# Optimization experiments

Hardware: AMD Instinct MI355X
Metric: run time of the kernel (lower is better)

## Reference

```python
import jax, jax.numpy as jnp
import numpy as np

B, S, D, H, R = 16, 2048, 1024, 1024, 16


def setup_inputs() -> dict:
    key = jax.random.key(0)
    ks = jax.random.split(key, 6)
    inv = 1.0 / np.sqrt(D)
    return {
        "x": jax.random.normal(ks[0], (B, S, D), jnp.float32),
        "Wa": jax.random.uniform(ks[1], (H, D), jnp.float32, -inv, inv),
        "ba": jnp.zeros((H,), jnp.float32),
        "Wg": jax.random.uniform(ks[2], (R, D), jnp.float32, -inv, inv),
        "bg": jnp.zeros((R,), jnp.float32),
        "Wu": jax.random.uniform(ks[3], (H, D), jnp.float32, -inv, inv),
        "bu": jnp.zeros((H,), jnp.float32),
        "u": jax.random.normal(ks[4], (H, R), jnp.float32) * 0.02,
        "v": jax.random.normal(ks[5], (H, R), jnp.float32) * 0.02,
    }


def reference(x, Wa, ba, Wg, bg, Wu, bu, u, v):
    # Precompute all per-step projections in big GEMMs (same math as the
    # per-step Linear calls in the original loop).
    a = jax.nn.sigmoid(jnp.einsum('bsd,hd->bsh', x, Wa) + ba)   # [B,S,H]
    g = jnp.einsum('bsd,rd->bsr', x, Wg) + bg                    # [B,S,R]
    u_in = jnp.einsum('bsd,hd->bsh', x, Wu) + bu                 # [B,S,H]

    def step(state, ins):
        a_t, g_t, u_t = ins                      # [B,H], [B,R], [B,H]
        low_rank = (state @ v) * g_t             # [B,R]
        state = a_t * state + u_t + low_rank @ u.T
        return state, None

    init = jnp.zeros((x.shape[0], Wa.shape[0]), x.dtype)
    seq = (jnp.swapaxes(a, 0, 1), jnp.swapaxes(g, 0, 1), jnp.swapaxes(u_in, 0, 1))
    state, _ = jax.lax.scan(step, init, seq)
    return state  # [B, H]
```

## Files before the change

kernel.cpp:

```cpp
#include <hip/hip_runtime.h>
#include <hip/hip_bf16.h>
#include <stdint.h>

#define Bb 16
#define Ss 2048
#define Dd 1024
#define Hh 1024
#define Rr 16
#define Mm 32768

typedef __attribute__((ext_vector_type(4))) float f32x4;
typedef __attribute__((ext_vector_type(8))) short bf16x8;
typedef __attribute__((ext_vector_type(2))) _Float16 h2;

__device__ __forceinline__ unsigned short f2bf(float f) {
    union { float f; uint32_t u; } c; c.f = f;
    uint32_t u = c.u + 0x7fffu + ((c.u >> 16) & 1u);
    return (unsigned short)(u >> 16);
}
__device__ __forceinline__ float bfbits2f(uint32_t bits) {
    union { uint32_t u; float f; } c; c.u = bits << 16; return c.f;
}
__device__ __forceinline__ h2 u2h(unsigned int x) {
    union { unsigned int u; h2 h; } c; c.u = x; return c.h;
}
__device__ __forceinline__ h2 mkh2(float a, float b) {
    h2 r; r.x = (_Float16)a; r.y = (_Float16)b; return r;
}

__device__ __forceinline__ float DOT2(h2 a, h2 b, float c) {
#if __has_builtin(__builtin_amdgcn_fdot2)
    return __builtin_amdgcn_fdot2(a, b, c, false);
#else
    return fmaf((float)a.x, (float)b.x, fmaf((float)a.y, (float)b.y, c));
#endif
}

__device__ __forceinline__ float dpp_xor8(float x) {
    return __int_as_float(__builtin_amdgcn_mov_dpp(
        __float_as_int(x), 0x128, 0xF, 0xF, false));
}
__device__ __forceinline__ float dpp_xor1(float x) {
    return __int_as_float(__builtin_amdgcn_mov_dpp(
        __float_as_int(x), 0xB1, 0xF, 0xF, false));
}

__device__ __forceinline__ void gld16(const void* gsrc, void* ldst) {
    __builtin_amdgcn_global_load_lds(
        (const __attribute__((address_space(1))) unsigned int*)gsrc,
        (__attribute__((address_space(3))) unsigned int*)ldst, 16, 0, 0);
}

__device__ __forceinline__ void softbar() {
    __asm volatile("" ::: "memory");
    __builtin_amdgcn_s_waitcnt(0xC07F);
    __builtin_amdgcn_s_barrier();
    __asm volatile("" ::: "memory");
}

__global__ __launch_bounds__(256) void k_convert(
    const float* __restrict__ x, const float* __restrict__ Wa,
    const float* __restrict__ Wu,
    unsigned short* __restrict__ xb, unsigned short* __restrict__ Wab,
    unsigned short* __restrict__ Wub)
{
    long e = ((long)blockIdx.x * 256 + threadIdx.x) * 4;
    const long nx = (long)Mm * Dd;
    const long nw = (long)Hh * Dd;
    const float* src; unsigned short* dst; long o;
    if (e < nx)            { src = x;  dst = xb;  o = e; }
    else if (e < nx + nw)  { src = Wa; dst = Wab; o = e - nx; }
    else                   { src = Wu; dst = Wub; o = e - nx - nw; }
    float4 f = *(const float4*)(src + o);
    ushort4 r;
    r.x = f2bf(f.x); r.y = f2bf(f.y); r.z = f2bf(f.z); r.w = f2bf(f.w);
    *(ushort4*)(dst + o) = r;
}

__global__ __launch_bounds__(256) void k_gemm(
    const unsigned short* __restrict__ Xb,
    const unsigned short* __restrict__ Wab,
    const unsigned short* __restrict__ Wub,
    const float* __restrict__ ba, const float* __restrict__ bu,
    unsigned short* __restrict__ outA, unsigned short* __restrict__ outU)
{
    __shared__ short At[128 * 32];
    __shared__ short Bt[128 * 32];

    const int tid  = threadIdx.x;
    const int lane = tid & 63;
    const int wave = tid >> 6;
    const int bm = blockIdx.x;
    const int bn = blockIdx.y;
    const int region = bn >> 3;
    const int nbase = (bn & 7) * 128;

    const short* Ag = (const short*)Xb;
    const short* Bg = (const short*)(region ? Wub : Wab);
    const float* bias = region ? bu : ba;
    unsigned short* outp = region ? outU : outA;

    const int wm = wave & 1, wn = wave >> 1;
    const int srow = lane >> 2, sseg = lane & 3;
    const int mrow = lane & 15, kb = lane >> 4;

    f32x4 acc[4][4] = {};

    for (int kt = 0; kt < 32; ++kt) {
        __syncthreads();
        const int k0 = kt * 32;
        #pragma unroll
        for (int p = 0; p < 2; ++p) {
            const int row = p * 64 + wave * 16 + srow;
            const short* ga = Ag + (long)(bm * 128 + row) * Dd + k0 + sseg * 8;
            gld16((const void*)ga, (void*)&At[p * 2048 + wave * 512]);
            const short* gb = Bg + (long)(nbase + row) * Dd + k0 + sseg * 8;
            gld16((const void*)gb, (void*)&Bt[p * 2048 + wave * 512]);
        }
        __syncthreads();

        bf16x8 af[4], bq[4];
        #pragma unroll
        for (int i = 0; i < 4; ++i) {
            af[i] = *(const bf16x8*)&At[(wm * 64 + i * 16 + mrow) * 32 + kb * 8];
            bq[i] = *(const bf16x8*)&Bt[(wn * 64 + i * 16 + mrow) * 32 + kb * 8];
        }
        #pragma unroll
        for (int i = 0; i < 4; ++i)
            #pragma unroll
            for (int j = 0; j < 4; ++j)
                acc[i][j] = __builtin_amdgcn_mfma_f32_16x16x32_bf16(
                    af[i], bq[j], acc[i][j], 0, 0, 0);
    }

    const int col = lane & 15, rq = lane >> 4;
    #pragma unroll
    for (int j = 0; j < 4; ++j) {
        const int n = nbase + wn * 64 + j * 16 + col;
        const float bv = bias[n];
        #pragma unroll
        for (int i = 0; i < 4; ++i) {
            const int mb = bm * 128 + wm * 64 + i * 16 + rq * 4;
            #pragma unroll
            for (int r = 0; r < 4; ++r) {
                float vv = acc[i][j][r] + bv;
                if (region == 0) vv = 1.0f / (1.0f + __expf(-vv));
                outp[(long)(mb + r) * Hh + n] = f2bf(vv);
            }
        }
    }
}

__global__ __launch_bounds__(256) void k_g(
    const float* __restrict__ x, const float* __restrict__ Wg,
    const float* __restrict__ bg, float* __restrict__ g)
{
    const int tid = threadIdx.x;
    const int r = tid & 15, ml = tid >> 4;
    const long m = (long)blockIdx.x * 16 + ml;
    const float4* xr = (const float4*)(x + m * Dd);
    const float4* wr = (const float4*)(Wg + (long)r * Dd);
    float acc = 0.0f;
    #pragma unroll 4
    for (int k = 0; k < Dd / 4; ++k) {
        float4 a = xr[k], b = wr[k];
        acc = fmaf(a.x, b.x, acc); acc = fmaf(a.y, b.y, acc);
        acc = fmaf(a.z, b.z, acc); acc = fmaf(a.w, b.w, acc);
    }
    g[m * Rr + r] = acc + bg[r];
}

__global__ __launch_bounds__(512) void k_scan(
    const unsigned short* __restrict__ a,
    const unsigned short* __restrict__ uin,
    const float* __restrict__ g,
    const float* __restrict__ u,
    const float* __restrict__ v,
    float* __restrict__ out)
{
    __shared__ __align__(16) _Float16 sh[Hh];
    __shared__ __align__(16) _Float16 cacc[16 * 8];
    __shared__ __align__(32) _Float16 qh[16];

    const int tid  = threadIdx.x;
    const int lane = tid & 63;
    const int wave = tid >> 6;
    const int oA   = lane >> 3;
    const int pA   = lane & 7;
    const int side = tid & 1;
    const int b = blockIdx.x;

    const int h0 = 2 * tid;
    const int hW = wave * 128 + oA * 16;
    h2 vrA[8], vrB[8];
    #pragma unroll
    for (int k = 0; k < 8; ++k) {
        vrA[k] = mkh2(v[(hW + 2 * k) * Rr + pA],
                      v[(hW + 2 * k + 1) * Rr + pA]);
        vrB[k] = mkh2(v[(hW + 2 * k) * Rr + pA + 8],
                      v[(hW + 2 * k + 1) * Rr + pA + 8]);
    }
    const int hp0 = 2 * (tid ^ 1);
    h2 ur00[4], ur01[4], urP0[4], urP1[4];
    #pragma unroll
    for (int k = 0; k < 4; ++k) {
        const int r0 = 8 * side + 2 * k;
        ur00[k] = mkh2(u[(h0)     * Rr + r0], u[(h0)     * Rr + r0 + 1]);
        ur01[k] = mkh2(u[(h0 + 1) * Rr + r0], u[(h0 + 1) * Rr + r0 + 1]);
        urP0[k] = mkh2(u[(hp0)     * Rr + r0], u[(hp0)     * Rr + r0 + 1]);
        urP1[k] = mkh2(u[(hp0 + 1) * Rr + r0], u[(hp0 + 1) * Rr + r0 + 1]);
    }

    const uint32_t* apu = (const uint32_t*)(a   + (long)b * Ss * Hh) + tid;
    const uint32_t* upu = (const uint32_t*)(uin + (long)b * Ss * Hh) + tid;
    const float*    gp  = g + (long)b * Ss * Rr + tid;

    float s0 = 0.0f, s1 = 0.0f;
    uint32_t pa[4], pu[4]; float pg[4];
    #pragma unroll
    for (int t = 0; t < 4; ++t) { pa[t] = apu[t * 512]; pu[t] = upu[t * 512]; }
    apu += 4 * 512; upu += 4 * 512;
    if (tid < 16) {
        #pragma unroll
        for (int t = 0; t < 4; ++t) pg[t] = gp[t * Rr];
        gp += 4 * Rr;
    }

    ((uint32_t*)sh)[tid] = 0u;
    __syncthreads();

    const _Float16* spA = &sh[hW];
    const _Float16* qpC = &qh[8 * side];
    const h2 one2 = mkh2(1.0f, 1.0f);

#define STEP(R, PF) do {                                                    \
           \
    uint4 sA = *(const uint4*)(spA);                                        \
    uint4 sB = *(const uint4*)(spA + 8);                                    \
    float lo, hi;                                                           \
    lo = DOT2(u2h(sA.x), vrA[0], 0.0f);                                     \
    lo = DOT2(u2h(sA.y), vrA[1], lo);                                       \
    lo = DOT2(u2h(sA.z), vrA[2], lo);                                       \
    lo = DOT2(u2h(sA.w), vrA[3], lo);                                       \
    lo = DOT2(u2h(sB.x), vrA[4], lo);                                       \
    lo = DOT2(u2h(sB.y), vrA[5], lo);                                       \
    lo = DOT2(u2h(sB.z), vrA[6], lo);                                       \
    lo = DOT2(u2h(sB.w), vrA[7], lo);                                       \
    hi = DOT2(u2h(sA.x), vrB[0], 0.0f);                                     \
    hi = DOT2(u2h(sA.y), vrB[1], hi);                                       \
    hi = DOT2(u2h(sA.z), vrB[2], hi);                                       \
    hi = DOT2(u2h(sA.w), vrB[3], hi);                                       \
    hi = DOT2(u2h(sB.x), vrB[4], hi);                                       \
    hi = DOT2(u2h(sB.y), vrB[5], hi);                                       \
    hi = DOT2(u2h(sB.z), vrB[6], hi);                                       \
    hi = DOT2(u2h(sB.w), vrB[7], hi);                                       \
     \
    {                                                                       \
        float tlo = dpp_xor8(lo), thi = dpp_xor8(hi);                       \
        float v1 = (lane & 8) ? (hi + thi) : (lo + tlo);                    \
        v1 += __shfl_xor(v1, 16);                                           \
        v1 += __shfl_xor(v1, 32);                                           \
        if (lane < 16) cacc[lane * 8 + wave] = (_Float16)v1;                \
    }                                                                       \
               \
    float a0 = bfbits2f(pa[R] & 0xFFFFu), a1 = bfbits2f(pa[R] >> 16);       \
    float u0 = bfbits2f(pu[R] & 0xFFFFu), u1 = bfbits2f(pu[R] >> 16);       \
    if (PF) {                                                               \
        pa[R] = *apu; apu += 512;                                           \
        pu[R] = *upu; upu += 512;                                           \
    }                                                                       \
    softbar();                                      \
               \
    if (tid < 16) {                                                         \
        uint4 c = *(const uint4*)&cacc[tid * 8];                            \
        float ssum;                                                         \
        ssum = DOT2(u2h(c.x), one2, 0.0f);                                  \
        ssum = DOT2(u2h(c.y), one2, ssum);                                  \
        ssum = DOT2(u2h(c.z), one2, ssum);                                  \
        ssum = DOT2(u2h(c.w), one2, ssum);                                  \
        qh[tid] = (_Float16)(pg[R] * ssum);                                 \
        if (PF) { pg[R] = *gp; gp += Rr; }                                  \
    }                                                                       \
    softbar();                                        \
     \
                 \
    uint4 q4 = *(const uint4*)qpC;                                          \
    h2 q0 = u2h(q4.x), q1 = u2h(q4.y), q2 = u2h(q4.z), q3 = u2h(q4.w);     \
    float pO0 = DOT2(q0, ur00[0],                                           \
                DOT2(q1, ur00[1], DOT2(q2, ur00[2], DOT2(q3, ur00[3], 0.0f))));\
    float pO1 = DOT2(q0, ur01[0],                                           \
                DOT2(q1, ur01[1], DOT2(q2, ur01[2], DOT2(q3, ur01[3], 0.0f))));\
    float pP0 = DOT2(q0, urP0[0],                                           \
                DOT2(q1, urP0[1], DOT2(q2, urP0[2], DOT2(q3, urP0[3], 0.0f))));\
    float pP1 = DOT2(q0, urP1[0],                                           \
                DOT2(q1, urP1[1], DOT2(q2, urP1[2], DOT2(q3, urP1[3], 0.0f))));\
    float lr0 = pO0 + dpp_xor1(pP0);                                        \
    float lr1 = pO1 + dpp_xor1(pP1);                                        \
    s0 = fmaf(a0, s0, u0 + lr0);                                            \
    s1 = fmaf(a1, s1, u1 + lr1);                                            \
    {                                                                       \
        union { _Float16 h[2]; uint32_t u32; } pk;                          \
        pk.h[0] = (_Float16)s0; pk.h[1] = (_Float16)s1;                     \
        ((uint32_t*)sh)[tid] = pk.u32;                                      \
    }                                                                       \
    softbar();                                     \
} while (0)

    for (int t4 = 0; t4 < Ss / 4 - 1; ++t4) {
        STEP(0, 1); STEP(1, 1); STEP(2, 1); STEP(3, 1);
    }
    STEP(0, 0); STEP(1, 0); STEP(2, 0); STEP(3, 0);
#undef STEP

    *(float2*)(out + (long)b * Hh + h0) = make_float2(s0, s1);
}

extern "C" void kernel_launch(void* const* d_in, const int* in_sizes, int n_in,
                              void* d_out, int out_size, void* d_ws, size_t ws_size,
                              hipStream_t stream)
{
    const float* x  = (const float*)d_in[0];
    const float* Wa = (const float*)d_in[1];
    const float* ba = (const float*)d_in[2];
    const float* Wg = (const float*)d_in[3];
    const float* bg = (const float*)d_in[4];
    const float* Wu = (const float*)d_in[5];
    const float* bu = (const float*)d_in[6];
    const float* u  = (const float*)d_in[7];
    const float* v  = (const float*)d_in[8];
    float* out = (float*)d_out;

    char* ws = (char*)d_ws;
    unsigned short* xb   = (unsigned short*)(ws);
    unsigned short* Wab  = (unsigned short*)(ws + 67108864);
    unsigned short* Wub  = (unsigned short*)(ws + 69206016);
    unsigned short* abuf = (unsigned short*)(ws + 71303168);
    unsigned short* ubuf = (unsigned short*)(ws + 138412032);
    float*          gbuf = (float*)(ws + 205520896);

    hipLaunchKernelGGL(k_convert, dim3(34816), dim3(256), 0, stream,
                       x, Wa, Wu, xb, Wab, Wub);
    hipLaunchKernelGGL(k_gemm, dim3(256, 16), dim3(256), 0, stream,
                       xb, Wab, Wub, ba, bu, abuf, ubuf);
    hipLaunchKernelGGL(k_g, dim3(2048), dim3(256), 0, stream,
                       x, Wg, bg, gbuf);
    hipLaunchKernelGGL(k_scan, dim3(Bb), dim3(512), 0, stream,
                       abuf, ubuf, gbuf, u, v, out);
}
```

Before: 1.858 ms.

## Restructure scan recurrence via precomputed K=vᵀu to cut one barrier per step

Precomputes K = vᵀu (16x16) in a tiny kernel and reformulates the recurrence so the rank-16 projection y of the new state is computed from the previous step's partial state plus K·q. This lets each step use a single block barrier with double-buffered shared state instead of three barriers. The q vector is broadcast via readlane instead of going through shared memory. This adds extra dot products per step and changes fp16 rounding behaviour. The K buffer reuses the start of the workspace, which also holds the bf16 copy of x.

```diff
diff --git a/kernel.cpp b/kernel.cpp
--- a/kernel.cpp
+++ b/kernel.cpp
@@ -27,6 +27,9 @@
 __device__ __forceinline__ h2 mkh2(float a, float b) {
     h2 r; r.x = (_Float16)a; r.y = (_Float16)b; return r;
 }
+__device__ __forceinline__ uint32_t h2u(h2 x) {
+    union { h2 h; uint32_t u; } c; c.h = x; return c.u;
+}
 
 __device__ __forceinline__ float DOT2(h2 a, h2 b, float c) {
 #if __has_builtin(__builtin_amdgcn_fdot2)
@@ -39,10 +42,6 @@
 __device__ __forceinline__ float dpp_xor8(float x) {
     return __int_as_float(__builtin_amdgcn_mov_dpp(
         __float_as_int(x), 0x128, 0xF, 0xF, false));
-}
-__device__ __forceinline__ float dpp_xor1(float x) {
-    return __int_as_float(__builtin_amdgcn_mov_dpp(
-        __float_as_int(x), 0xB1, 0xF, 0xF, false));
 }
 
 __device__ __forceinline__ void gld16(const void* gsrc, void* ldst) {
@@ -170,147 +169,151 @@
     g[m * Rr + r] = acc + bg[r];
 }
 
+__global__ __launch_bounds__(256) void k_K(
+    const float* __restrict__ u, const float* __restrict__ v,
+    float* __restrict__ Kbuf)
+{
+    const int r = threadIdx.x >> 4;
+    const int c = threadIdx.x & 15;
+    float acc = 0.0f;
+    for (int h = 0; h < Hh; ++h)
+        acc = fmaf(v[h * Rr + r], u[h * Rr + c], acc);
+    Kbuf[r * 16 + c] = acc;
+}
+
 __global__ __launch_bounds__(512) void k_scan(
     const unsigned short* __restrict__ a,
     const unsigned short* __restrict__ uin,
     const float* __restrict__ g,
     const float* __restrict__ u,
     const float* __restrict__ v,
+    const float* __restrict__ Kbuf,
     float* __restrict__ out)
 {
-    __shared__ __align__(16) _Float16 sh[Hh];
-    __shared__ __align__(16) _Float16 cacc[16 * 8];
-    __shared__ __align__(32) _Float16 qh[16];
+    __shared__ __align__(16) h2 shad[2][512];
+    __shared__ __align__(16) _Float16 cacc[2][16][8];
 
     const int tid  = threadIdx.x;
     const int lane = tid & 63;
     const int wave = tid >> 6;
     const int oA   = lane >> 3;
     const int pA   = lane & 7;
-    const int side = tid & 1;
-    const int b = blockIdx.x;
-
-    const int h0 = 2 * tid;
+    const int ra   = lane & 15;
+    const int b    = blockIdx.x;
+    const int h0   = 2 * tid;
+
     const int hW = wave * 128 + oA * 16;
     h2 vrA[8], vrB[8];
     #pragma unroll
     for (int k = 0; k < 8; ++k) {
-        vrA[k] = mkh2(v[(hW + 2 * k) * Rr + pA],
-                      v[(hW + 2 * k + 1) * Rr + pA]);
-        vrB[k] = mkh2(v[(hW + 2 * k) * Rr + pA + 8],
-                      v[(hW + 2 * k + 1) * Rr + pA + 8]);
-    }
-    const int hp0 = 2 * (tid ^ 1);
-    h2 ur00[4], ur01[4], urP0[4], urP1[4];
+        vrA[k] = mkh2(v[(hW + 2*k) * Rr + pA],
+                      v[(hW + 2*k + 1) * Rr + pA]);
+        vrB[k] = mkh2(v[(hW + 2*k) * Rr + pA + 8],
+                      v[(hW + 2*k + 1) * Rr + pA + 8]);
+    }
+    h2 ur0[8], ur1[8], kr[8];
     #pragma unroll
-    for (int k = 0; k < 4; ++k) {
-        const int r0 = 8 * side + 2 * k;
-        ur00[k] = mkh2(u[(h0)     * Rr + r0], u[(h0)     * Rr + r0 + 1]);
-        ur01[k] = mkh2(u[(h0 + 1) * Rr + r0], u[(h0 + 1) * Rr + r0 + 1]);
-        urP0[k] = mkh2(u[(hp0)     * Rr + r0], u[(hp0)     * Rr + r0 + 1]);
-        urP1[k] = mkh2(u[(hp0 + 1) * Rr + r0], u[(hp0 + 1) * Rr + r0 + 1]);
+    for (int j = 0; j < 8; ++j) {
+        ur0[j] = mkh2(u[h0 * Rr + j],        u[h0 * Rr + j + 8]);
+        ur1[j] = mkh2(u[(h0 + 1) * Rr + j],  u[(h0 + 1) * Rr + j + 8]);
+        kr[j]  = mkh2(Kbuf[ra * 16 + j],     Kbuf[ra * 16 + j + 8]);
     }
 
     const uint32_t* apu = (const uint32_t*)(a   + (long)b * Ss * Hh) + tid;
     const uint32_t* upu = (const uint32_t*)(uin + (long)b * Ss * Hh) + tid;
-    const float*    gp  = g + (long)b * Ss * Rr + tid;
-
-    float s0 = 0.0f, s1 = 0.0f;
-    uint32_t pa[4], pu[4]; float pg[4];
-    #pragma unroll
-    for (int t = 0; t < 4; ++t) { pa[t] = apu[t * 512]; pu[t] = upu[t * 512]; }
-    apu += 4 * 512; upu += 4 * 512;
-    if (tid < 16) {
-        #pragma unroll
-        for (int t = 0; t < 4; ++t) pg[t] = gp[t * Rr];
-        gp += 4 * Rr;
-    }
-
-    ((uint32_t*)sh)[tid] = 0u;
+    const float*    gp  = g + (long)b * Ss * Rr + ra;
+
+    float s0 = 0.0f, s1 = 0.0f, y = 0.0f;
+
+    uint32_t pa_[4], pu_[4]; float pg_[4];
+    pa_[2] = apu[1*512]; pa_[3] = apu[2*512]; pa_[0] = apu[3*512]; pa_[1] = apu[4*512];
+    pu_[2] = upu[1*512]; pu_[3] = upu[2*512]; pu_[0] = upu[3*512]; pu_[1] = upu[4*512];
+    uint32_t u0r = upu[0];
+    apu += 5 * 512; upu += 5 * 512;
+    pg_[1] = gp[0]; pg_[2] = gp[Rr]; pg_[3] = gp[2*Rr]; pg_[0] = gp[3*Rr];
+    gp += 4 * Rr;
+
+    float tA = bfbits2f(u0r & 0xFFFFu);
+    float tB = bfbits2f(u0r >> 16);
+    shad[1][tid] = mkh2(tA, tB);
     __syncthreads();
 
-    const _Float16* spA = &sh[hW];
-    const _Float16* qpC = &qh[8 * side];
     const h2 one2 = mkh2(1.0f, 1.0f);
 
-#define STEP(R, PF) do {                                                    \
-           \
-    uint4 sA = *(const uint4*)(spA);                                        \
-    uint4 sB = *(const uint4*)(spA + 8);                                    \
+#define BODY(RG, RA, PAR, PF) do {                                          \
+             \
+    uint4 w0 = *(const uint4*)&shad[PAR][wave * 64 + oA * 8];               \
+    uint4 w1 = *(const uint4*)&shad[PAR][wave * 64 + oA * 8 + 4];           \
+       \
+    float q = pg_[RG] * y;                                                  \
+    float qo = dpp_xor8(q);                                                 \
+    uint32_t qpk = h2u(mkh2(q, qo));                                        \
+    uint32_t qv[8];                                                         \
+    qv[0] = (uint32_t)__builtin_amdgcn_readlane((int)qpk, 0);               \
+    qv[1] = (uint32_t)__builtin_amdgcn_readlane((int)qpk, 1);               \
+    qv[2] = (uint32_t)__builtin_amdgcn_readlane((int)qpk, 2);               \
+    qv[3] = (uint32_t)__builtin_amdgcn_readlane((int)qpk, 3);               \
+    qv[4] = (uint32_t)__builtin_amdgcn_readlane((int)qpk, 4);               \
+    qv[5] = (uint32_t)__builtin_amdgcn_readlane((int)qpk, 5);               \
+    qv[6] = (uint32_t)__builtin_amdgcn_readlane((int)qpk, 6);               \
+    qv[7] = (uint32_t)__builtin_amdgcn_readlane((int)qpk, 7);               \
+                                                   \
+    float lr0, lr1;                                                         \
+    lr0 = DOT2(u2h(qv[0]), ur0[0], 0.0f);                                   \
+    lr0 = DOT2(u2h(qv[1]), ur0[1], lr0); lr0 = DOT2(u2h(qv[2]), ur0[2], lr0);\
+    lr0 = DOT2(u2h(qv[3]), ur0[3], lr0); lr0 = DOT2(u2h(qv[4]), ur0[4], lr0);\
+    lr0 = DOT2(u2h(qv[5]), ur0[5], lr0); lr0 = DOT2(u2h(qv[6]), ur0[6], lr0);\
+    lr0 = DOT2(u2h(qv[7]), ur0[7], lr0);                                    \
+    lr1 = DOT2(u2h(qv[0]), ur1[0], 0.0f);                                   \
+    lr1 = DOT2(u2h(qv[1]), ur1[1], lr1); lr1 = DOT2(u2h(qv[2]), ur1[2], lr1);\
+    lr1 = DOT2(u2h(qv[3]), ur1[3], lr1); lr1 = DOT2(u2h(qv[4]), ur1[4], lr1);\
+    lr1 = DOT2(u2h(qv[5]), ur1[5], lr1); lr1 = DOT2(u2h(qv[6]), ur1[6], lr1);\
+    lr1 = DOT2(u2h(qv[7]), ur1[7], lr1);                                    \
+    s0 = tA + lr0; s1 = tB + lr1;                                           \
+                             \
+    float na0 = bfbits2f(pa_[RA] & 0xFFFFu), na1 = bfbits2f(pa_[RA] >> 16); \
+    float nu0 = bfbits2f(pu_[RA] & 0xFFFFu), nu1 = bfbits2f(pu_[RA] >> 16); \
+    tA = fmaf(na0, s0, nu0); tB = fmaf(na1, s1, nu1);                       \
+    shad[PAR ^ 1][tid] = mkh2(tA, tB);                                      \
+    if (PF) { pa_[RA] = *apu; apu += 512; pu_[RA] = *upu; upu += 512;       \
+              pg_[RG] = *gp; gp += Rr; }                                    \
+                                \
     float lo, hi;                                                           \
-    lo = DOT2(u2h(sA.x), vrA[0], 0.0f);                                     \
-    lo = DOT2(u2h(sA.y), vrA[1], lo);                                       \
-    lo = DOT2(u2h(sA.z), vrA[2], lo);                                       \
-    lo = DOT2(u2h(sA.w), vrA[3], lo);                                       \
-    lo = DOT2(u2h(sB.x), vrA[4], lo);                                       \
-    lo = DOT2(u2h(sB.y), vrA[5], lo);                                       \
-    lo = DOT2(u2h(sB.z), vrA[6], lo);                                       \
-    lo = DOT2(u2h(sB.w), vrA[7], lo);                                       \
-    hi = DOT2(u2h(sA.x), vrB[0], 0.0f);                                     \
-    hi = DOT2(u2h(sA.y), vrB[1], hi);                                       \
-    hi = DOT2(u2h(sA.z), vrB[2], hi);                                       \
-    hi = DOT2(u2h(sA.w), vrB[3], hi);                                       \
-    hi = DOT2(u2h(sB.x), vrB[4], hi);                                       \
-    hi = DOT2(u2h(sB.y), vrB[5], hi);                                       \
-    hi = DOT2(u2h(sB.z), vrB[6], hi);                                       \
-    hi = DOT2(u2h(sB.w), vrB[7], hi);                                       \
-     \
+    lo = DOT2(u2h(w0.x), vrA[0], 0.0f); lo = DOT2(u2h(w0.y), vrA[1], lo);   \
+    lo = DOT2(u2h(w0.z), vrA[2], lo);   lo = DOT2(u2h(w0.w), vrA[3], lo);   \
+    lo = DOT2(u2h(w1.x), vrA[4], lo);   lo = DOT2(u2h(w1.y), vrA[5], lo);   \
+    lo = DOT2(u2h(w1.z), vrA[6], lo);   lo = DOT2(u2h(w1.w), vrA[7], lo);   \
+    hi = DOT2(u2h(w0.x), vrB[0], 0.0f); hi = DOT2(u2h(w0.y), vrB[1], hi);   \
+    hi = DOT2(u2h(w0.z), vrB[2], hi);   hi = DOT2(u2h(w0.w), vrB[3], hi);   \
+    hi = DOT2(u2h(w1.x), vrB[4], hi);   hi = DOT2(u2h(w1.y), vrB[5], hi);   \
+    hi = DOT2(u2h(w1.z), vrB[6], hi);   hi = DOT2(u2h(w1.w), vrB[7], hi);   \
     {                                                                       \
         float tlo = dpp_xor8(lo), thi = dpp_xor8(hi);                       \
         float v1 = (lane & 8) ? (hi + thi) : (lo + tlo);                    \
         v1 += __shfl_xor(v1, 16);                                           \
         v1 += __shfl_xor(v1, 32);                                           \
-        if (lane < 16) cacc[lane * 8 + wave] = (_Float16)v1;                \
-    }                                                                       \
-               \
-    float a0 = bfbits2f(pa[R] & 0xFFFFu), a1 = bfbits2f(pa[R] >> 16);       \
-    float u0 = bfbits2f(pu[R] & 0xFFFFu), u1 = bfbits2f(pu[R] >> 16);       \
-    if (PF) {                                                               \
-        pa[R] = *apu; apu += 512;                                           \
-        pu[R] = *upu; upu += 512;                                           \
+        if (lane < 16) cacc[PAR][lane][wave] = (_Float16)v1;                \
     }                                                                       \
     softbar();                                      \
-               \
-    if (tid < 16) {                                                         \
-        uint4 c = *(const uint4*)&cacc[tid * 8];                            \
-        float ssum;                                                         \
-        ssum = DOT2(u2h(c.x), one2, 0.0f);                                  \
-        ssum = DOT2(u2h(c.y), one2, ssum);                                  \
-        ssum = DOT2(u2h(c.z), one2, ssum);                                  \
-        ssum = DOT2(u2h(c.w), one2, ssum);                                  \
-        qh[tid] = (_Float16)(pg[R] * ssum);                                 \
-        if (PF) { pg[R] = *gp; gp += Rr; }                                  \
-    }                                                                       \
-    softbar();                                        \
-     \
-                 \
-    uint4 q4 = *(const uint4*)qpC;                                          \
-    h2 q0 = u2h(q4.x), q1 = u2h(q4.y), q2 = u2h(q4.z), q3 = u2h(q4.w);     \
-    float pO0 = DOT2(q0, ur00[0],                                           \
-                DOT2(q1, ur00[1], DOT2(q2, ur00[2], DOT2(q3, ur00[3], 0.0f))));\
-    float pO1 = DOT2(q0, ur01[0],                                           \
-                DOT2(q1, ur01[1], DOT2(q2, ur01[2], DOT2(q3, ur01[3], 0.0f))));\
-    float pP0 = DOT2(q0, urP0[0],                                           \
-                DOT2(q1, urP0[1], DOT2(q2, urP0[2], DOT2(q3, urP0[3], 0.0f))));\
-    float pP1 = DOT2(q0, urP1[0],                                           \
-                DOT2(q1, urP1[1], DOT2(q2, urP1[2], DOT2(q3, urP1[3], 0.0f))));\
-    float lr0 = pO0 + dpp_xor1(pP0);                                        \
-    float lr1 = pO1 + dpp_xor1(pP1);                                        \
-    s0 = fmaf(a0, s0, u0 + lr0);                                            \
-    s1 = fmaf(a1, s1, u1 + lr1);                                            \
-    {                                                                       \
-        union { _Float16 h[2]; uint32_t u32; } pk;                          \
-        pk.h[0] = (_Float16)s0; pk.h[1] = (_Float16)s1;                     \
-        ((uint32_t*)sh)[tid] = pk.u32;                                      \
-    }                                                                       \
-    softbar();                                     \
+                                                 \
+    uint4 c4 = *(const uint4*)&cacc[PAR][ra][0];                            \
+    float wf;                                                               \
+    wf = DOT2(u2h(c4.x), one2, 0.0f); wf = DOT2(u2h(c4.y), one2, wf);       \
+    wf = DOT2(u2h(c4.z), one2, wf);   wf = DOT2(u2h(c4.w), one2, wf);       \
+    float ky;                                                               \
+    ky = DOT2(u2h(qv[0]), kr[0], 0.0f);                                     \
+    ky = DOT2(u2h(qv[1]), kr[1], ky); ky = DOT2(u2h(qv[2]), kr[2], ky);     \
+    ky = DOT2(u2h(qv[3]), kr[3], ky); ky = DOT2(u2h(qv[4]), kr[4], ky);     \
+    ky = DOT2(u2h(qv[5]), kr[5], ky); ky = DOT2(u2h(qv[6]), kr[6], ky);     \
+    ky = DOT2(u2h(qv[7]), kr[7], ky);                                       \
+    y = wf + ky;                                                            \
 } while (0)
 
-    for (int t4 = 0; t4 < Ss / 4 - 1; ++t4) {
-        STEP(0, 1); STEP(1, 1); STEP(2, 1); STEP(3, 1);
-    }
-    STEP(0, 0); STEP(1, 0); STEP(2, 0); STEP(3, 0);
-#undef STEP
+    for (int t4 = 0; t4 < 511; ++t4) {
+        BODY(1, 2, 1, 1); BODY(2, 3, 0, 1); BODY(3, 0, 1, 1); BODY(0, 1, 0, 1);
+    }
+    BODY(1, 2, 1, 0); BODY(2, 3, 0, 0); BODY(3, 0, 1, 0); BODY(0, 1, 0, 0);
+#undef BODY
 
     *(float2*)(out + (long)b * Hh + h0) = make_float2(s0, s1);
 }
@@ -337,13 +340,15 @@
     unsigned short* abuf = (unsigned short*)(ws + 71303168);
     unsigned short* ubuf = (unsigned short*)(ws + 138412032);
     float*          gbuf = (float*)(ws + 205520896);
+    float*          Kbuf = (float*)(ws);
 
     hipLaunchKernelGGL(k_convert, dim3(34816), dim3(256), 0, stream,
                        x, Wa, Wu, xb, Wab, Wub);
     hipLaunchKernelGGL(k_gemm, dim3(256, 16), dim3(256), 0, stream,
                        xb, Wab, Wub, ba, bu, abuf, ubuf);
+    hipLaunchKernelGGL(k_K, dim3(1), dim3(256), 0, stream, u, v, Kbuf);
     hipLaunchKernelGGL(k_g, dim3(2048), dim3(256), 0, stream,
                        x, Wg, bg, gbuf);
     hipLaunchKernelGGL(k_scan, dim3(Bb), dim3(512), 0, stream,
-                       abuf, ubuf, gbuf, u, v, out);
-}
+                       abuf, ubuf, gbuf, u, v, Kbuf, out);
+}
```

Result: faster. 1.591 ms (-14.4%).
